# Performance work log

Measured on AMD Instinct MI355X. Metric: run time of the kernel, lower is better.

The kernel has to match this reference:

```python
import jax, jax.numpy as jnp
import numpy as np

N = 4096
IN_DIM = 256
H = 4        # n_heads
D = 64       # head_dim (out_dim)
NEG_SLOPE = 0.2


def setup_inputs() -> dict:
    key = jax.random.key(0)
    k_h, k_adj, k_zero, k_W, k_a = jax.random.split(key, 5)
    h = jax.random.normal(k_h, (N, IN_DIM), dtype=jnp.float32)
    adj = jax.random.normal(k_adj, (N, N), dtype=jnp.float32)
    keep = jax.random.uniform(k_zero, (N, N)) >= 0.3
    adj_bias = jnp.where(keep, adj, 0.0)
    W = jax.random.normal(k_W, (IN_DIM, H * D), dtype=jnp.float32) * 0.05
    a = jax.random.normal(k_a, (H, 2 * D), dtype=jnp.float32) * 0.05
    return {"h": h, "adj_bias": adj_bias, "W": W, "a": a}


def reference(h, adj_bias, W, a):
    n = h.shape[0]
    Wh = (h @ W).reshape(n, H, D)                       # [N, H, D]
    # (cat([Wh_i, Wh_j]) * a).sum(-1) separates into two rank-1 terms:
    a_i, a_j = a[:, :D], a[:, D:]                       # [H, D] each
    e_i = jnp.einsum('nhd,hd->nh', Wh, a_i)             # score from dest node i
    e_j = jnp.einsum('nhd,hd->nh', Wh, a_j)             # score from src node j
    e = jax.nn.leaky_relu(e_i[:, None, :] + e_j[None, :, :], NEG_SLOPE)  # [N,N,H]
    mask = (adj_bias == 0.0)[:, :, None]                # [N, N, 1]
    e = e + adj_bias[:, :, None]
    e = jnp.where(mask, -jnp.inf, e)
    # rows where every neighbor is masked: force self-loop score 0
    all_masked = jnp.all(mask, axis=1, keepdims=True)   # [N, 1, 1]
    self_loop = jnp.eye(n, dtype=bool)[:, :, None]      # [N, N, 1]
    e = jnp.where(all_masked & self_loop, 0.0, e)
    alpha = jax.nn.softmax(e, axis=1)                   # softmax over sources j
    # dropout: eval mode (p acts as identity), faithful to training=False
    out = jnp.einsum('ijh,jhd->ihd', alpha, Wh).reshape(n, H * D)  # concat heads
    return jax.nn.elu(out)
```

## Files before the change

kernel.cpp:

```cpp
#include <hip/hip_runtime.h>
#include <cstdint>
#include <cstddef>


typedef _Float16 f16x4 __attribute__((ext_vector_type(4)));
typedef _Float16 f16x8 __attribute__((ext_vector_type(8)));
typedef float f32x4 __attribute__((ext_vector_type(4)));

#define NN 4096

__global__ __launch_bounds__(256) void gemm_wh(
    const float* __restrict__ A, const float* __restrict__ Bw,
    const float* __restrict__ av, float* __restrict__ C,
    _Float16* __restrict__ Vt,
    _Float16* __restrict__ uit, _Float16* __restrict__ ui5t,
    _Float16* __restrict__ ujt, _Float16* __restrict__ uj5t) {
  __shared__ float sA[32][36];
  __shared__ float sB[32][68];
  __shared__ _Float16 sT[64][40];
  const int h  = blockIdx.x;
  const int by = blockIdx.y;
  const int t  = threadIdx.x;
  const int row0 = by * 32, col0 = h * 64;
  const int tc = t & 15, tr = t >> 4;
  float acc[2][4];
  #pragma unroll
  for (int q = 0; q < 2; q++)
    #pragma unroll
    for (int p = 0; p < 4; p++) acc[q][p] = 0.f;

  for (int k0 = 0; k0 < 256; k0 += 32) {
    __syncthreads();
    {
      const int r = t >> 3, k4 = (t & 7) * 4;
      float4 v = *(const float4*)&A[(size_t)(row0 + r) * 256 + k0 + k4];
      sA[k4 + 0][r] = v.x; sA[k4 + 1][r] = v.y;
      sA[k4 + 2][r] = v.z; sA[k4 + 3][r] = v.w;
    }
    #pragma unroll
    for (int q = 0; q < 2; q++) {
      const int u = t + q * 256;
      const int kr = u >> 4, c4 = (u & 15) * 4;
      *(float4*)&sB[kr][c4] =
          *(const float4*)&Bw[(size_t)(k0 + kr) * 256 + col0 + c4];
    }
    __syncthreads();
    #pragma unroll
    for (int kk = 0; kk < 32; kk++) {
      float2 a2 = *(const float2*)&sA[kk][tr * 2];
      float4 bv = *(const float4*)&sB[kk][tc * 4];
      const float bp[4] = {bv.x, bv.y, bv.z, bv.w};
      #pragma unroll
      for (int p = 0; p < 4; p++) {
        acc[0][p] = fmaf(a2.x, bp[p], acc[0][p]);
        acc[1][p] = fmaf(a2.y, bp[p], acc[1][p]);
      }
    }
  }
  #pragma unroll
  for (int q = 0; q < 2; q++) {
    float4 v = make_float4(acc[q][0], acc[q][1], acc[q][2], acc[q][3]);
    *(float4*)&C[(size_t)(row0 + tr * 2 + q) * 256 + col0 + tc * 4] = v;
  }
  {
    float pi[2] = {0.f, 0.f}, pj[2] = {0.f, 0.f};
    #pragma unroll
    for (int q = 0; q < 2; q++)
      #pragma unroll
      for (int p = 0; p < 4; p++) {
        const int d = tc * 4 + p;
        pi[q] = fmaf(acc[q][p], av[h * 128 + d], pi[q]);
        pj[q] = fmaf(acc[q][p], av[h * 128 + 64 + d], pj[q]);
      }
    #pragma unroll
    for (int m = 1; m <= 8; m <<= 1) {
      #pragma unroll
      for (int q = 0; q < 2; q++) {
        pi[q] += __shfl_xor(pi[q], m, 64);
        pj[q] += __shfl_xor(pj[q], m, 64);
      }
    }
    if (tc == 0) {
      #pragma unroll
      for (int q = 0; q < 2; q++) {
        const int row = row0 + tr * 2 + q;
        uit [(size_t)h * NN + row] = (_Float16)__expf(0.2f * pi[q]);
        ui5t[(size_t)h * NN + row] = (_Float16)__expf(pi[q]);
        ujt [(size_t)h * NN + row] = (_Float16)__expf(0.2f * pj[q]);
        uj5t[(size_t)h * NN + row] = (_Float16)__expf(pj[q]);
      }
    }
  }
  #pragma unroll
  for (int q = 0; q < 2; q++)
    #pragma unroll
    for (int p = 0; p < 4; p++)
      sT[tc * 4 + p][tr * 2 + q] = (_Float16)acc[q][p];
  __syncthreads();
  {
    const int dd = t >> 2, j8 = (t & 3) * 8;
    f16x8 w;
    #pragma unroll
    for (int k = 0; k < 8; k++) w[k] = sT[dd][j8 + k];
    *(f16x8*)&Vt[(size_t)(col0 + dd) * NN + row0 + j8] = w;
  }
}

__global__ __launch_bounds__(256, 4) void gat_attn(
    const float* __restrict__ bias, const _Float16* __restrict__ Vt,
    const _Float16* __restrict__ uit, const _Float16* __restrict__ ui5t,
    const _Float16* __restrict__ ujt, const _Float16* __restrict__ uj5t,
    float* __restrict__ P, float* __restrict__ L, int jpc) {
  __shared__ _Float16 seb[2][32][136];
  const int itile = blockIdx.x;
  const int chunk = blockIdx.y;
  const int tid = threadIdx.x;
  const int lane = tid & 63;
  const int h = __builtin_amdgcn_readfirstlane(tid >> 6);
  const int m = lane & 15;
  const int quad = lane >> 4;
  const int i0 = itile * 32;
  const int j0 = chunk * jpc;
  const int nc = jpc >> 7;

  f32x4 acc[2][5];
  #pragma unroll
  for (int it = 0; it < 2; it++)
    #pragma unroll
    for (int dt = 0; dt < 5; dt++)
      #pragma unroll
      for (int r = 0; r < 4; r++) acc[it][dt][r] = 0.f;

  const _Float16 ui_0 = uit [(size_t)h * NN + i0 + m];
  const _Float16 ui_1 = uit [(size_t)h * NN + i0 + 16 + m];
  const _Float16 u5_0 = ui5t[(size_t)h * NN + i0 + m];
  const _Float16 u5_1 = ui5t[(size_t)h * NN + i0 + 16 + m];
  const f16x8 ui8_0 = {ui_0, ui_0, ui_0, ui_0, ui_0, ui_0, ui_0, ui_0};
  const f16x8 ui8_1 = {ui_1, ui_1, ui_1, ui_1, ui_1, ui_1, ui_1, ui_1};
  const f16x8 u58_0 = {u5_0, u5_0, u5_0, u5_0, u5_0, u5_0, u5_0, u5_0};
  const f16x8 u58_1 = {u5_1, u5_1, u5_1, u5_1, u5_1, u5_1, u5_1, u5_1};
  const f16x8 kOne = {(_Float16)1.f, (_Float16)1.f, (_Float16)1.f, (_Float16)1.f,
                      (_Float16)1.f, (_Float16)1.f, (_Float16)1.f, (_Float16)1.f};

  auto stage = [&](int jc, int buf) {
    const int r = tid >> 3, f = tid & 7;
    const float* bp = bias + (size_t)(i0 + r) * NN + j0 + jc * 128;
    #pragma unroll
    for (int q = 0; q < 4; q++) {
      float4 v = *(const float4*)(bp + f * 4 + q * 32);
      f16x4 e;
      e[0] = (_Float16)((v.x == 0.f) ? 0.f : __expf(v.x));
      e[1] = (_Float16)((v.y == 0.f) ? 0.f : __expf(v.y));
      e[2] = (_Float16)((v.z == 0.f) ? 0.f : __expf(v.z));
      e[3] = (_Float16)((v.w == 0.f) ? 0.f : __expf(v.w));
      *(f16x4*)&seb[buf][r][f * 4 + q * 32] = e;
    }
  };

  stage(0, 0);
  for (int jc = 0; jc < nc; jc++) {
    const int buf = jc & 1;
    __syncthreads();
    if (jc + 1 < nc) stage(jc + 1, buf ^ 1);

    const _Float16* vb  = Vt + (size_t)(h * 64 + m) * NN + j0 + jc * 128 + quad * 8;
    const _Float16* ujb = ujt  + (size_t)h * NN + j0 + jc * 128 + quad * 8;
    const _Float16* u5b = uj5t + (size_t)h * NN + j0 + jc * 128 + quad * 8;

    f16x8 bc[4], bn[4];
    #pragma unroll
    for (int dt = 0; dt < 4; dt++)
      bc[dt] = *(const f16x8*)(vb + (size_t)(dt * 16) * NN);

    #pragma unroll
    for (int s = 0; s < 4; s++) {
      if (s < 3) {
        #pragma unroll
        for (int dt = 0; dt < 4; dt++)
          bn[dt] = *(const f16x8*)(vb + (size_t)(dt * 16) * NN + (s + 1) * 32);
      }
      const f16x8 uj8  = *(const f16x8*)(ujb + s * 32);
      const f16x8 uj58 = *(const f16x8*)(u5b + s * 32);
      const f16x8 e0 = *(const f16x8*)&seb[buf][m][s * 32 + quad * 8];
      const f16x8 e1 = *(const f16x8*)&seb[buf][m + 16][s * 32 + quad * 8];
      const f16x8 a0 = e0 * __builtin_elementwise_max(u58_0 * uj58, ui8_0 * uj8);
      const f16x8 a1 = e1 * __builtin_elementwise_max(u58_1 * uj58, ui8_1 * uj8);
      #pragma unroll
      for (int dt = 0; dt < 4; dt++) {
        acc[0][dt] = __builtin_amdgcn_mfma_f32_16x16x32_f16(a0, bc[dt], acc[0][dt], 0, 0, 0);
        acc[1][dt] = __builtin_amdgcn_mfma_f32_16x16x32_f16(a1, bc[dt], acc[1][dt], 0, 0, 0);
      }
      acc[0][4] = __builtin_amdgcn_mfma_f32_16x16x32_f16(a0, kOne, acc[0][4], 0, 0, 0);
      acc[1][4] = __builtin_amdgcn_mfma_f32_16x16x32_f16(a1, kOne, acc[1][4], 0, 0, 0);
      if (s < 3) {
        #pragma unroll
        for (int dt = 0; dt < 4; dt++) bc[dt] = bn[dt];
      }
    }
  }

  const size_t lb = (size_t)(chunk * 4 + h) * NN + i0;
  if (m == 0) {
    #pragma unroll
    for (int it = 0; it < 2; it++)
      #pragma unroll
      for (int r = 0; r < 4; r++)
        L[lb + it * 16 + quad * 4 + r] = acc[it][4][r];
  }
  const size_t pbase = ((size_t)(chunk * 4 + h) * NN + i0) * 64;
  #pragma unroll
  for (int it = 0; it < 2; it++)
    #pragma unroll
    for (int dt = 0; dt < 4; dt++)
      #pragma unroll
      for (int r = 0; r < 4; r++)
        P[pbase + (size_t)(it * 16 + quad * 4 + r) * 64 + dt * 16 + m] = acc[it][dt][r];
}

template <int CHT>
__global__ __launch_bounds__(256) void reduce_out(
    const float* __restrict__ P, const float* __restrict__ L,
    const float* __restrict__ Wh, float* __restrict__ out) {
  const int i0 = blockIdx.x * 16;
  const int h = blockIdx.y;
  const int t = threadIdx.x;
  const int d = t & 63;
  const int isub = t >> 6;
  #pragma unroll
  for (int ii = 0; ii < 4; ii++) {
    const int i = i0 + isub * 4 + ii;
    float lsum = 0.f, s = 0.f;
    #pragma unroll
    for (int c = 0; c < CHT; c++) {
      lsum += L[(size_t)(c * 4 + h) * NN + i];
      s += P[((size_t)(c * 4 + h) * NN + i) * 64 + d];
    }
    const float wh = Wh[(size_t)i * 256 + h * 64 + d];
    const bool fb = (lsum == 0.f);
    float o = fb ? wh : s / lsum;
    o = (o > 0.f) ? o : (__expf(o) - 1.f);
    out[(size_t)i * 256 + h * 64 + d] = o;
  }
}

extern "C" void kernel_launch(void* const* d_in, const int* in_sizes, int n_in,
                              void* d_out, int out_size, void* d_ws, size_t ws_size,
                              hipStream_t stream) {
  const float* h_in = (const float*)d_in[0];
  const float* adj  = (const float*)d_in[1];
  const float* W    = (const float*)d_in[2];
  const float* a    = (const float*)d_in[3];
  float* out = (float*)d_out;
  float* ws = (float*)d_ws;

  int CH = 8;
  while (CH > 1) {
    size_t floats = 1048576  + 524288  + 32768  +
                    (size_t)CH * (16384 + 1048576);
    if (floats * 4 <= ws_size) break;
    CH >>= 1;
  }
  const int jpc = NN / CH;

  float* Wh = ws;
  _Float16* Vt   = (_Float16*)(ws + 1048576);
  _Float16* uit  = (_Float16*)(ws + 1048576 + 524288);
  _Float16* ui5t = uit + 16384;
  _Float16* ujt  = ui5t + 16384;
  _Float16* uj5t = ujt + 16384;
  float* Lb = ws + 1048576 + 524288 + 32768;
  float* Pb = Lb + (size_t)CH * 16384;

  hipLaunchKernelGGL(gemm_wh, dim3(4, 128), dim3(256), 0, stream,
                     h_in, W, a, Wh, Vt, uit, ui5t, ujt, uj5t);
  hipLaunchKernelGGL(gat_attn, dim3(128, CH), dim3(256), 0, stream,
                     adj, Vt, uit, ui5t, ujt, uj5t, Pb, Lb, jpc);
  switch (CH) {
    case 8: hipLaunchKernelGGL((reduce_out<8>), dim3(256, 4), dim3(256), 0, stream, Pb, Lb, Wh, out); break;
    case 4: hipLaunchKernelGGL((reduce_out<4>), dim3(256, 4), dim3(256), 0, stream, Pb, Lb, Wh, out); break;
    case 2: hipLaunchKernelGGL((reduce_out<2>), dim3(256, 4), dim3(256), 0, stream, Pb, Lb, Wh, out); break;
    default: hipLaunchKernelGGL((reduce_out<1>), dim3(256, 4), dim3(256), 0, stream, Pb, Lb, Wh, out); break;
  }
}
```

Measured before the change: 155.1 us.

## Halve attention row tile to 16 and prefetch bias into registers before LDS fill

The attention kernel now handles 16 destination rows per block instead of 32, doubling the grid and raising the occupancy hint to 8 blocks per SM. This cuts accumulator registers and LDS per block. The bias staging is split into a global load issued early into registers and an exp-and-store into LDS after the MFMA loop, so load latency overlaps compute. In exchange, each Vt fragment loaded from global is reused for only one row tile instead of two, roughly doubling V traffic per output row.

After: 281.7 us. 1.82x slower.

```diff
diff --git a/kernel.cpp b/kernel.cpp
--- a/kernel.cpp
+++ b/kernel.cpp
@@ -106,12 +106,12 @@
   }
 }
 
-__global__ __launch_bounds__(256, 4) void gat_attn(
+__global__ __launch_bounds__(256, 8) void gat_attn(
     const float* __restrict__ bias, const _Float16* __restrict__ Vt,
     const _Float16* __restrict__ uit, const _Float16* __restrict__ ui5t,
     const _Float16* __restrict__ ujt, const _Float16* __restrict__ uj5t,
     float* __restrict__ P, float* __restrict__ L, int jpc) {
-  __shared__ _Float16 seb[2][32][136];
+  __shared__ _Float16 seb[2][16][136];
   const int itile = blockIdx.x;
   const int chunk = blockIdx.y;
   const int tid = threadIdx.x;
@@ -119,49 +119,52 @@
   const int h = __builtin_amdgcn_readfirstlane(tid >> 6);
   const int m = lane & 15;
   const int quad = lane >> 4;
-  const int i0 = itile * 32;
+  const int i0 = itile * 16;
   const int j0 = chunk * jpc;
   const int nc = jpc >> 7;
 
-  f32x4 acc[2][5];
-  #pragma unroll
-  for (int it = 0; it < 2; it++)
-    #pragma unroll
-    for (int dt = 0; dt < 5; dt++)
-      #pragma unroll
-      for (int r = 0; r < 4; r++) acc[it][dt][r] = 0.f;
-
-  const _Float16 ui_0 = uit [(size_t)h * NN + i0 + m];
-  const _Float16 ui_1 = uit [(size_t)h * NN + i0 + 16 + m];
-  const _Float16 u5_0 = ui5t[(size_t)h * NN + i0 + m];
-  const _Float16 u5_1 = ui5t[(size_t)h * NN + i0 + 16 + m];
-  const f16x8 ui8_0 = {ui_0, ui_0, ui_0, ui_0, ui_0, ui_0, ui_0, ui_0};
-  const f16x8 ui8_1 = {ui_1, ui_1, ui_1, ui_1, ui_1, ui_1, ui_1, ui_1};
-  const f16x8 u58_0 = {u5_0, u5_0, u5_0, u5_0, u5_0, u5_0, u5_0, u5_0};
-  const f16x8 u58_1 = {u5_1, u5_1, u5_1, u5_1, u5_1, u5_1, u5_1, u5_1};
+  f32x4 acc[5];
+  #pragma unroll
+  for (int dt = 0; dt < 5; dt++)
+    #pragma unroll
+    for (int r = 0; r < 4; r++) acc[dt][r] = 0.f;
+
+  const _Float16 ui_v = uit [(size_t)h * NN + i0 + m];
+  const _Float16 u5_v = ui5t[(size_t)h * NN + i0 + m];
+  const f16x8 ui8 = {ui_v, ui_v, ui_v, ui_v, ui_v, ui_v, ui_v, ui_v};
+  const f16x8 u58 = {u5_v, u5_v, u5_v, u5_v, u5_v, u5_v, u5_v, u5_v};
   const f16x8 kOne = {(_Float16)1.f, (_Float16)1.f, (_Float16)1.f, (_Float16)1.f,
                       (_Float16)1.f, (_Float16)1.f, (_Float16)1.f, (_Float16)1.f};
 
-  auto stage = [&](int jc, int buf) {
-    const int r = tid >> 3, f = tid & 7;
-    const float* bp = bias + (size_t)(i0 + r) * NN + j0 + jc * 128;
-    #pragma unroll
-    for (int q = 0; q < 4; q++) {
-      float4 v = *(const float4*)(bp + f * 4 + q * 32);
-      f16x4 e;
-      e[0] = (_Float16)((v.x == 0.f) ? 0.f : __expf(v.x));
-      e[1] = (_Float16)((v.y == 0.f) ? 0.f : __expf(v.y));
-      e[2] = (_Float16)((v.z == 0.f) ? 0.f : __expf(v.z));
-      e[3] = (_Float16)((v.w == 0.f) ? 0.f : __expf(v.w));
-      *(f16x4*)&seb[buf][r][f * 4 + q * 32] = e;
-    }
+  const int sr = tid >> 4, sf = tid & 15;
+  const float* bp0 = bias + (size_t)(i0 + sr) * NN + j0 + sf * 4;
+  float4 pf0, pf1;
+  auto load_chunk = [&](int jc) {
+    const float* bp = bp0 + jc * 128;
+    pf0 = *(const float4*)(bp);
+    pf1 = *(const float4*)(bp + 64);
   };
-
-  stage(0, 0);
+  auto fill = [&](int buf) {
+    f16x4 e0v, e1v;
+    e0v[0] = (_Float16)((pf0.x == 0.f) ? 0.f : __expf(pf0.x));
+    e0v[1] = (_Float16)((pf0.y == 0.f) ? 0.f : __expf(pf0.y));
+    e0v[2] = (_Float16)((pf0.z == 0.f) ? 0.f : __expf(pf0.z));
+    e0v[3] = (_Float16)((pf0.w == 0.f) ? 0.f : __expf(pf0.w));
+    e1v[0] = (_Float16)((pf1.x == 0.f) ? 0.f : __expf(pf1.x));
+    e1v[1] = (_Float16)((pf1.y == 0.f) ? 0.f : __expf(pf1.y));
+    e1v[2] = (_Float16)((pf1.z == 0.f) ? 0.f : __expf(pf1.z));
+    e1v[3] = (_Float16)((pf1.w == 0.f) ? 0.f : __expf(pf1.w));
+    *(f16x4*)&seb[buf][sr][sf * 4] = e0v;
+    *(f16x4*)&seb[buf][sr][sf * 4 + 64] = e1v;
+  };
+
+  load_chunk(0);
+  fill(0);
+
   for (int jc = 0; jc < nc; jc++) {
     const int buf = jc & 1;
     __syncthreads();
-    if (jc + 1 < nc) stage(jc + 1, buf ^ 1);
+    if (jc + 1 < nc) load_chunk(jc + 1);
 
     const _Float16* vb  = Vt + (size_t)(h * 64 + m) * NN + j0 + jc * 128 + quad * 8;
     const _Float16* ujb = ujt  + (size_t)h * NN + j0 + jc * 128 + quad * 8;
@@ -182,39 +185,31 @@
       const f16x8 uj8  = *(const f16x8*)(ujb + s * 32);
       const f16x8 uj58 = *(const f16x8*)(u5b + s * 32);
       const f16x8 e0 = *(const f16x8*)&seb[buf][m][s * 32 + quad * 8];
-      const f16x8 e1 = *(const f16x8*)&seb[buf][m + 16][s * 32 + quad * 8];
-      const f16x8 a0 = e0 * __builtin_elementwise_max(u58_0 * uj58, ui8_0 * uj8);
-      const f16x8 a1 = e1 * __builtin_elementwise_max(u58_1 * uj58, ui8_1 * uj8);
-      #pragma unroll
-      for (int dt = 0; dt < 4; dt++) {
-        acc[0][dt] = __builtin_amdgcn_mfma_f32_16x16x32_f16(a0, bc[dt], acc[0][dt], 0, 0, 0);
-        acc[1][dt] = __builtin_amdgcn_mfma_f32_16x16x32_f16(a1, bc[dt], acc[1][dt], 0, 0, 0);
-      }
-      acc[0][4] = __builtin_amdgcn_mfma_f32_16x16x32_f16(a0, kOne, acc[0][4], 0, 0, 0);
-      acc[1][4] = __builtin_amdgcn_mfma_f32_16x16x32_f16(a1, kOne, acc[1][4], 0, 0, 0);
+      const f16x8 a0 = e0 * __builtin_elementwise_max(u58 * uj58, ui8 * uj8);
+      #pragma unroll
+      for (int dt = 0; dt < 4; dt++)
+        acc[dt] = __builtin_amdgcn_mfma_f32_16x16x32_f16(a0, bc[dt], acc[dt], 0, 0, 0);
+      acc[4] = __builtin_amdgcn_mfma_f32_16x16x32_f16(a0, kOne, acc[4], 0, 0, 0);
       if (s < 3) {
         #pragma unroll
         for (int dt = 0; dt < 4; dt++) bc[dt] = bn[dt];
       }
     }
+    if (jc + 1 < nc) fill(buf ^ 1);
   }
 
   const size_t lb = (size_t)(chunk * 4 + h) * NN + i0;
   if (m == 0) {
     #pragma unroll
-    for (int it = 0; it < 2; it++)
-      #pragma unroll
-      for (int r = 0; r < 4; r++)
-        L[lb + it * 16 + quad * 4 + r] = acc[it][4][r];
+    for (int r = 0; r < 4; r++)
+      L[lb + quad * 4 + r] = acc[4][r];
   }
   const size_t pbase = ((size_t)(chunk * 4 + h) * NN + i0) * 64;
   #pragma unroll
-  for (int it = 0; it < 2; it++)
-    #pragma unroll
-    for (int dt = 0; dt < 4; dt++)
-      #pragma unroll
-      for (int r = 0; r < 4; r++)
-        P[pbase + (size_t)(it * 16 + quad * 4 + r) * 64 + dt * 16 + m] = acc[it][dt][r];
+  for (int dt = 0; dt < 4; dt++)
+    #pragma unroll
+    for (int r = 0; r < 4; r++)
+      P[pbase + (size_t)(quad * 4 + r) * 64 + dt * 16 + m] = acc[dt][r];
 }
 
 template <int CHT>
@@ -273,7 +268,7 @@
 
   hipLaunchKernelGGL(gemm_wh, dim3(4, 128), dim3(256), 0, stream,
                      h_in, W, a, Wh, Vt, uit, ui5t, ujt, uj5t);
-  hipLaunchKernelGGL(gat_attn, dim3(128, CH), dim3(256), 0, stream,
+  hipLaunchKernelGGL(gat_attn, dim3(256, CH), dim3(256), 0, stream,
                      adj, Vt, uit, ui5t, ujt, uj5t, Pb, Lb, jpc);
   switch (CH) {
     case 8: hipLaunchKernelGGL((reduce_out<8>), dim3(256, 4), dim3(256), 0, stream, Pb, Lb, Wh, out); break;
```
